# Kernel optimization log

Measured on AMD Instinct MI355X. Metric: run time of the kernel, lower is better.

Reference implementation:

```python
import jax, jax.numpy as jnp
import numpy as np

N = 50000        # nodes
E = 800000       # edges
F_IN = 16        # num_features
F_EDGE = 8       # num_edge_features
H = 4            # heads
C = 32           # hidden_dim (per-head out channels)
D = H * C        # 128, node state width
NUM_CLASSES = 5
NEG_SLOPE = 0.2  # PyG GATConv default leaky_relu slope


def setup_inputs() -> dict:
    key = jax.random.key(0)
    ks = jax.random.split(key, 30)
    def w(k, shape):
        return jax.random.normal(k, shape, dtype=jnp.float32) * 0.05
    return {
        "x": jax.random.normal(ks[0], (N, F_IN), dtype=jnp.float32),
        "edge_index": jax.random.randint(ks[1], (2, E), 0, N),
        "edge_attr": jax.random.normal(ks[2], (E, F_EDGE), dtype=jnp.float32),
        # edge_encoder: Linear(F_EDGE->C), ReLU, Linear(C->H)
        "ee_w1": w(ks[3], (C, F_EDGE)), "ee_b1": jnp.zeros((C,), jnp.float32),
        "ee_w2": w(ks[4], (H, C)),      "ee_b2": jnp.zeros((H,), jnp.float32),
        # input_proj: Linear(F_IN -> D)
        "proj_w": w(ks[5], (D, F_IN)), "proj_b": jnp.zeros((D,), jnp.float32),
        # conv1: GATConv(F_IN, C, heads=H, edge_dim=H, concat=True)
        "c1_lin": w(ks[6], (D, F_IN)),
        "c1_att_src": w(ks[7], (H, C)), "c1_att_dst": w(ks[8], (H, C)),
        "c1_lin_edge": w(ks[9], (D, H)), "c1_att_edge": w(ks[10], (H, C)),
        "c1_bias": jnp.zeros((D,), jnp.float32),
        # conv2: GATConv(D, C, heads=H, edge_dim=H, concat=True)
        "c2_lin": w(ks[11], (D, D)),
        "c2_att_src": w(ks[12], (H, C)), "c2_att_dst": w(ks[13], (H, C)),
        "c2_lin_edge": w(ks[14], (D, H)), "c2_att_edge": w(ks[15], (H, C)),
        "c2_bias": jnp.zeros((D,), jnp.float32),
        # layer norms
        "n1_g": jnp.ones((D,), jnp.float32), "n1_b": jnp.zeros((D,), jnp.float32),
        "n2_g": jnp.ones((D,), jnp.float32), "n2_b": jnp.zeros((D,), jnp.float32),
        # jk_proj: Linear(3D -> D)
        "jk_w": w(ks[16], (D, 3 * D)), "jk_b": jnp.zeros((D,), jnp.float32),
        # classifier: Linear(D -> NUM_CLASSES)
        "cls_w": w(ks[17], (NUM_CLASSES, D)), "cls_b": jnp.zeros((NUM_CLASSES,), jnp.float32),
    }


def _layer_norm(h, g, b, eps=1e-5):
    mu = jnp.mean(h, axis=-1, keepdims=True)
    var = jnp.var(h, axis=-1, keepdims=True)
    return (h - mu) * jax.lax.rsqrt(var + eps) * g + b


def _gat_conv(x, src, dst, e_attr, lin_w, att_src, att_dst, lin_edge_w, att_edge, bias):
    """PyG GATConv (v1) with edge features, concat=True, eval mode (no dropout)."""
    n = x.shape[0]
    xs = (x @ lin_w.T).reshape(n, H, C)                      # [N,H,C]
    a_src = jnp.einsum('nhc,hc->nh', xs, att_src)            # [N,H]
    a_dst = jnp.einsum('nhc,hc->nh', xs, att_dst)            # [N,H]
    ee = (e_attr @ lin_edge_w.T).reshape(-1, H, C)           # [E,H,C]
    a_edge = jnp.einsum('ehc,hc->eh', ee, att_edge)          # [E,H]
    alpha = jax.nn.leaky_relu(a_src[src] + a_dst[dst] + a_edge, NEG_SLOPE)
    # segment softmax over destination neighborhoods
    amax = jax.ops.segment_max(alpha, dst, num_segments=n)
    ex = jnp.exp(alpha - amax[dst])
    denom = jax.ops.segment_sum(ex, dst, num_segments=n)
    alpha = ex / (denom[dst] + 1e-16)                        # [E,H]
    msg = xs[src] * alpha[:, :, None]                        # [E,H,C]
    out = jax.ops.segment_sum(msg, dst, num_segments=n)      # [N,H,C]
    return out.reshape(n, H * C) + bias


def reference(x, edge_index, edge_attr,
              ee_w1, ee_b1, ee_w2, ee_b2,
              proj_w, proj_b,
              c1_lin, c1_att_src, c1_att_dst, c1_lin_edge, c1_att_edge, c1_bias,
              c2_lin, c2_att_src, c2_att_dst, c2_lin_edge, c2_att_edge, c2_bias,
              n1_g, n1_b, n2_g, n2_b,
              jk_w, jk_b, cls_w, cls_b):
    src, dst = edge_index[0], edge_index[1]
    # edge encoder
    e = jax.nn.relu(edge_attr @ ee_w1.T + ee_b1) @ ee_w2.T + ee_b2   # [E,H]
    h0 = x @ proj_w.T + proj_b                                        # [N,D]
    h1 = _gat_conv(x, src, dst, e, c1_lin, c1_att_src, c1_att_dst,
                   c1_lin_edge, c1_att_edge, c1_bias)
    h1 = _layer_norm(jax.nn.elu(h1) + h0, n1_g, n1_b)
    h2 = _gat_conv(h1, src, dst, e, c2_lin, c2_att_src, c2_att_dst,
                   c2_lin_edge, c2_att_edge, c2_bias)
    h2 = _layer_norm(jax.nn.elu(h2) + h1, n2_g, n2_b)
    h = jnp.concatenate([h0, h1, h2], axis=-1) @ jk_w.T + jk_b
    out = h @ cls_w.T + cls_b
    return jax.nn.log_softmax(out, axis=1)
```

## Files before the change

### kernel.cpp

```cpp
#include <hip/hip_runtime.h>
#include <cstdint>

#define NN 50000
#define NE 800000
#define DPX 6250
#define SLICES 391

using short8  = __attribute__((ext_vector_type(8))) short;
using float4v = __attribute__((ext_vector_type(4))) float;

__device__ __forceinline__ ushort f2bf(float f) {
    uint u = __float_as_uint(f);
    uint r = (u + 0x7fffu + ((u >> 16) & 1u)) >> 16;
    return (ushort)r;
}
__device__ __forceinline__ float bf2f(uint u) {
    return __uint_as_float(u << 16);
}

__global__ __launch_bounds__(256) void k_prep2(const float* __restrict__ le1, const float* __restrict__ ae1,
                                               const float* __restrict__ le2, const float* __restrict__ ae2,
                                               const float* __restrict__ jkw, const float* __restrict__ jkb,
                                               const float* __restrict__ clw, const float* __restrict__ clb,
                                               const float* __restrict__ projw, const float* __restrict__ c1lin,
                                               const float* __restrict__ c2lin,
                                               const float* __restrict__ asrc1, const float* __restrict__ adst1,
                                               float* __restrict__ M, float* __restrict__ CW,
                                               float* __restrict__ cbp,
                                               ushort* __restrict__ w01b, ushort* __restrict__ c2b,
                                               float* __restrict__ Vmat, int* __restrict__ deg)
{
    int idx = blockIdx.x * 256 + threadIdx.x;
    if (idx < NN) deg[idx] = 0;
    if (idx < 32) {
        const float* le = (idx < 16) ? le1 : le2;
        const float* ae = (idx < 16) ? ae1 : ae2;
        int hk = idx & 15, h = hk >> 2, k = hk & 3;
        float s = 0.f;
        for (int c = 0; c < 32; ++c)
            s += le[(h * 32 + c) * 4 + k] * ae[h * 32 + c];
        M[idx] = s;
    } else if (idx < 1952) {
        int o = idx - 32;
        int r = o / 384, c = o - r * 384;
        float s = 0.f;
        for (int k = 0; k < 128; ++k)
            s += clw[r * 128 + k] * jkw[(size_t)k * 384 + c];
        CW[o] = s;
    } else if (idx < 1957) {
        int r = idx - 1952;
        float s = clb[r];
        for (int k = 0; k < 128; ++k)
            s += clw[r * 128 + k] * jkb[k];
        cbp[r] = s;
    } else if (idx >= 2048 && idx < 10240) {
        int o = idx - 2048;
        int r = o >> 5, c = o & 31;
        float v = 0.f;
        if (c < 16) v = (r < 128) ? projw[r * 16 + c] : c1lin[(r - 128) * 16 + c];
        w01b[o] = f2bf(v);
    } else if (idx >= 10240 && idx < 26624) {
        int o = idx - 10240;
        c2b[o] = f2bf(c2lin[o]);
    } else if (idx >= 26624 && idx < 26752) {
        int o = idx - 26624;
        const float* att = (o < 64) ? asrc1 : adst1;
        int oo = o & 63, h = oo >> 4, k = oo & 15;
        float s = 0.f;
        for (int c = 0; c < 32; ++c)
            s += c1lin[(h * 32 + c) * 16 + k] * att[h * 32 + c];
        Vmat[o] = s;
    }
}

__global__ __launch_bounds__(256) void k_att1(const float* __restrict__ x,
                                              const float* __restrict__ V,
                                              float* __restrict__ as_o,
                                              float* __restrict__ ad_o)
{
    __shared__ float sV[128];
    int t = threadIdx.x;
    if (t < 128) sV[t] = V[t];
    __syncthreads();
    int n = blockIdx.x * 256 + t;
    if (n >= NN) return;
    const float4* xr = (const float4*)(x + (size_t)n * 16);
    float4 x0 = xr[0], x1 = xr[1], x2 = xr[2], x3 = xr[3];
    float xv[16] = {x0.x,x0.y,x0.z,x0.w, x1.x,x1.y,x1.z,x1.w,
                    x2.x,x2.y,x2.z,x2.w, x3.x,x3.y,x3.z,x3.w};
    float s[4], d[4];
    #pragma unroll
    for (int h = 0; h < 4; ++h) {
        float ss = 0.f, dd = 0.f;
        #pragma unroll
        for (int k = 0; k < 16; ++k) {
            ss += xv[k] * sV[h * 16 + k];
            dd += xv[k] * sV[64 + h * 16 + k];
        }
        s[h] = ss; d[h] = dd;
    }
    *(float4*)(as_o + (size_t)n * 4) = make_float4(s[0], s[1], s[2], s[3]);
    *(float4*)(ad_o + (size_t)n * 4) = make_float4(d[0], d[1], d[2], d[3]);
}

__global__ __launch_bounds__(256) void k_edge_mlp(const float* __restrict__ ea,
                                                  const float* __restrict__ w1,
                                                  const float* __restrict__ b1,
                                                  const float* __restrict__ w2,
                                                  const float* __restrict__ b2,
                                                  const int* __restrict__ ei,
                                                  const float* __restrict__ Mm,
                                                  const float* __restrict__ as1,
                                                  const float* __restrict__ ad1,
                                                  ushort* __restrict__ exb,
                                                  ushort* __restrict__ ae2)
{
    __shared__ float sw1[256], sb1[32], sw2[128], sb2[4], sM[32];
    int t = threadIdx.x;
    sw1[t] = w1[t];
    if (t < 128) sw2[t] = w2[t];
    if (t < 32)  { sb1[t] = b1[t]; sM[t] = Mm[t]; }
    if (t < 4)   sb2[t] = b2[t];
    __syncthreads();
    int e = blockIdx.x * 256 + t;
    if (e >= NE) return;
    int src = ei[e], dst = ei[NE + e];
    float4 s4 = *(const float4*)(as1 + (size_t)src * 4);
    float4 d4 = *(const float4*)(ad1 + (size_t)dst * 4);
    float4 x0 = *(const float4*)(ea + (size_t)e * 8);
    float4 x1 = *(const float4*)(ea + (size_t)e * 8 + 4);
    float o0 = sb2[0], o1 = sb2[1], o2 = sb2[2], o3 = sb2[3];
    #pragma unroll
    for (int j = 0; j < 32; ++j) {
        const float* w = sw1 + j * 8;
        float s = sb1[j] + w[0]*x0.x + w[1]*x0.y + w[2]*x0.z + w[3]*x0.w
                         + w[4]*x1.x + w[5]*x1.y + w[6]*x1.z + w[7]*x1.w;
        s = fmaxf(s, 0.f);
        o0 += sw2[0*32+j] * s; o1 += sw2[1*32+j] * s;
        o2 += sw2[2*32+j] * s; o3 += sw2[3*32+j] * s;
    }
    float sa[4] = {s4.x, s4.y, s4.z, s4.w};
    float da[4] = {d4.x, d4.y, d4.z, d4.w};
    ushort exq[4], a2q[4];
    #pragma unroll
    for (int h = 0; h < 4; ++h) {
        float ae1 = sM[h*4+0]*o0 + sM[h*4+1]*o1 + sM[h*4+2]*o2 + sM[h*4+3]*o3;
        float al = sa[h] + da[h] + ae1;
        al = al > 0.f ? al : 0.2f * al;
        exq[h] = f2bf(__expf(al));
        a2q[h] = f2bf(sM[16+h*4+0]*o0 + sM[16+h*4+1]*o1 + sM[16+h*4+2]*o2 + sM[16+h*4+3]*o3);
    }
    *(uint2*)(exb + (size_t)e * 4) =
        make_uint2((uint)exq[0] | ((uint)exq[1] << 16), (uint)exq[2] | ((uint)exq[3] << 16));
    *(uint2*)(ae2 + (size_t)e * 4) =
        make_uint2((uint)a2q[0] | ((uint)a2q[1] << 16), (uint)a2q[2] | ((uint)a2q[3] << 16));
}

__global__ __launch_bounds__(256) void k_hist8(const int* __restrict__ ei, int* __restrict__ deg)
{
    int grp = blockIdx.x & 7;
    int base = (blockIdx.x >> 3) * 2048 + threadIdx.x;
    #pragma unroll
    for (int k = 0; k < 8; ++k) {
        int e = base + k * 256;
        if (e < NE) {
            int dst = ei[NE + e];
            if (dst / DPX == grp) atomicAdd(&deg[dst], 1);
        }
    }
}

__global__ __launch_bounds__(256) void k_scan_blk(const int* __restrict__ deg,
                                                  int* __restrict__ loc,
                                                  int* __restrict__ bsum)
{
    __shared__ int tmp[256];
    int t = threadIdx.x;
    int i = blockIdx.x * 256 + t;
    int v = (i < NN) ? deg[i] : 0;
    tmp[t] = v;
    __syncthreads();
    #pragma unroll
    for (int o = 1; o < 256; o <<= 1) {
        int add = (t >= o) ? tmp[t - o] : 0;
        __syncthreads();
        tmp[t] += add;
        __syncthreads();
    }
    if (i < NN) loc[i] = tmp[t] - v;
    if (t == 255) bsum[blockIdx.x] = tmp[255];
}

__global__ __launch_bounds__(256) void k_scan_top(const int* __restrict__ bsum,
                                                  int* __restrict__ bcarry,
                                                  int* __restrict__ total_out, int nb)
{
    __shared__ int tmp[256];
    int t = threadIdx.x;
    int v = (t < nb) ? bsum[t] : 0;
    tmp[t] = v;
    __syncthreads();
    #pragma unroll
    for (int o = 1; o < 256; o <<= 1) {
        int add = (t >= o) ? tmp[t - o] : 0;
        __syncthreads();
        tmp[t] += add;
        __syncthreads();
    }
    if (t < nb) bcarry[t] = tmp[t] - v;
    if (t == 255) *total_out = tmp[255];
}

__global__ __launch_bounds__(256) void k_scan_add(const int* __restrict__ loc,
                                                  const int* __restrict__ bcarry,
                                                  int* __restrict__ off,
                                                  int* __restrict__ cur)
{
    int i = blockIdx.x * 256 + threadIdx.x;
    if (i < NN) {
        int o = loc[i] + bcarry[blockIdx.x];
        off[i] = o;
        cur[i] = o;
    }
}

__global__ __launch_bounds__(256) void k_scatter8(const int* __restrict__ ei,
                                                  int* __restrict__ cursor,
                                                  int2* __restrict__ csr2)
{
    int grp = blockIdx.x & 7;
    int base = (blockIdx.x >> 3) * 2048 + threadIdx.x;
    #pragma unroll
    for (int k = 0; k < 8; ++k) {
        int e = base + k * 256;
        if (e < NE) {
            int dst = ei[NE + e];
            if (dst / DPX == grp) {
                int src = ei[e];
                int p = atomicAdd(&cursor[dst], 1);
                csr2[p] = make_int2(src, e);
            }
        }
    }
}

__global__ __launch_bounds__(256) void k_gemm1(const float* __restrict__ x,
                                               const ushort* __restrict__ w01,
                                               const float* __restrict__ pbias,
                                               ushort* __restrict__ hcatb,
                                               ushort* __restrict__ xs, int M)
{
    int t = threadIdx.x;
    int wv = t >> 6, lane = t & 63;
    int quad = lane >> 4, r16 = lane & 15;
    int m0 = blockIdx.x * 128 + wv * 32;
    int ar0 = m0 + r16;      if (ar0 >= M) ar0 = M - 1;
    int ar1 = m0 + 16 + r16; if (ar1 >= M) ar1 = M - 1;
    short8 a0 = (short8){0,0,0,0,0,0,0,0}, a1 = a0;
    if (quad < 2) {
        const float* p0 = x + (size_t)ar0 * 16 + quad * 8;
        const float* p1 = x + (size_t)ar1 * 16 + quad * 8;
        float4 u0 = *(const float4*)p0, u1 = *(const float4*)(p0 + 4);
        float4 v0 = *(const float4*)p1, v1 = *(const float4*)(p1 + 4);
        a0[0]=(short)f2bf(u0.x); a0[1]=(short)f2bf(u0.y); a0[2]=(short)f2bf(u0.z); a0[3]=(short)f2bf(u0.w);
        a0[4]=(short)f2bf(u1.x); a0[5]=(short)f2bf(u1.y); a0[6]=(short)f2bf(u1.z); a0[7]=(short)f2bf(u1.w);
        a1[0]=(short)f2bf(v0.x); a1[1]=(short)f2bf(v0.y); a1[2]=(short)f2bf(v0.z); a1[3]=(short)f2bf(v0.w);
        a1[4]=(short)f2bf(v1.x); a1[5]=(short)f2bf(v1.y); a1[6]=(short)f2bf(v1.z); a1[7]=(short)f2bf(v1.w);
    }
    float4v acc[2][16];
    #pragma unroll
    for (int i = 0; i < 2; ++i)
        #pragma unroll
        for (int j = 0; j < 16; ++j) acc[i][j] = (float4v){0.f, 0.f, 0.f, 0.f};
    #pragma unroll
    for (int nt = 0; nt < 16; ++nt) {
        short8 b = *(const short8*)(w01 + (size_t)(nt * 16 + r16) * 32 + quad * 8);
        acc[0][nt] = __builtin_amdgcn_mfma_f32_16x16x32_bf16(a0, b, acc[0][nt], 0, 0, 0);
        acc[1][nt] = __builtin_amdgcn_mfma_f32_16x16x32_bf16(a1, b, acc[1][nt], 0, 0, 0);
    }
    #pragma unroll
    for (int rt = 0; rt < 2; ++rt) {
        #pragma unroll
        for (int nt = 0; nt < 16; ++nt) {
            int col = (nt & 7) * 16 + r16;
            float bv = (nt < 8) ? pbias[col] : 0.f;
            #pragma unroll
            for (int r = 0; r < 4; ++r) {
                int row = m0 + rt * 16 + quad * 4 + r;
                if (row < M) {
                    float v = acc[rt][nt][r] + bv;
                    if (nt < 8) hcatb[(size_t)row * 384 + col] = f2bf(v);
                    else        xs[(size_t)row * 128 + col] = f2bf(v);
                }
            }
        }
    }
}

__global__ __launch_bounds__(256) void k_gemm2(const ushort* __restrict__ A,
                                               const ushort* __restrict__ W,
                                               const float* __restrict__ atts,
                                               const float* __restrict__ attd,
                                               ushort* __restrict__ xs,
                                               float* __restrict__ as_o,
                                               float* __restrict__ ad_o, int M)
{
    __shared__ float sAs[128], sAd[128];
    int t = threadIdx.x;
    if (t < 128) { sAs[t] = atts[t]; sAd[t] = attd[t]; }
    __syncthreads();
    int wv = t >> 6, lane = t & 63;
    int quad = lane >> 4, r16 = lane & 15;
    int m0 = blockIdx.x * 128 + wv * 32;
    float4v acc[2][8];
    #pragma unroll
    for (int i = 0; i < 2; ++i)
        #pragma unroll
        for (int j = 0; j < 8; ++j) acc[i][j] = (float4v){0.f, 0.f, 0.f, 0.f};
    int ar0 = m0 + r16;      if (ar0 >= M) ar0 = M - 1;
    int ar1 = m0 + 16 + r16; if (ar1 >= M) ar1 = M - 1;
    const ushort* a0p = A + (size_t)ar0 * 384 + quad * 8;
    const ushort* a1p = A + (size_t)ar1 * 384 + quad * 8;
    const ushort* wp  = W + (size_t)r16 * 128 + quad * 8;
    #pragma unroll
    for (int k0 = 0; k0 < 128; k0 += 32) {
        short8 a0 = *(const short8*)(a0p + k0);
        short8 a1 = *(const short8*)(a1p + k0);
        #pragma unroll
        for (int nt = 0; nt < 8; ++nt) {
            short8 b = *(const short8*)(wp + (size_t)(nt * 16) * 128 + k0);
            acc[0][nt] = __builtin_amdgcn_mfma_f32_16x16x32_bf16(a0, b, acc[0][nt], 0, 0, 0);
            acc[1][nt] = __builtin_amdgcn_mfma_f32_16x16x32_bf16(a1, b, acc[1][nt], 0, 0, 0);
        }
    }
    #pragma unroll
    for (int rt = 0; rt < 2; ++rt) {
        #pragma unroll
        for (int nt = 0; nt < 8; ++nt) {
            int col = nt * 16 + r16;
            #pragma unroll
            for (int r = 0; r < 4; ++r) {
                int row = m0 + rt * 16 + quad * 4 + r;
                if (row < M)
                    xs[(size_t)row * 128 + col] = f2bf(acc[rt][nt][r]);
            }
        }
        #pragma unroll
        for (int r = 0; r < 4; ++r) {
            int row = m0 + rt * 16 + quad * 4 + r;
            float sh[4], dh[4];
            #pragma unroll
            for (int h = 0; h < 4; ++h) {
                int cA = h * 32 + r16, cB = cA + 16;
                sh[h] = acc[rt][2*h][r] * sAs[cA] + acc[rt][2*h+1][r] * sAs[cB];
                dh[h] = acc[rt][2*h][r] * sAd[cA] + acc[rt][2*h+1][r] * sAd[cB];
            }
            #pragma unroll
            for (int o = 1; o < 16; o <<= 1) {
                #pragma unroll
                for (int h = 0; h < 4; ++h) {
                    sh[h] += __shfl_xor(sh[h], o, 64);
                    dh[h] += __shfl_xor(dh[h], o, 64);
                }
            }
            if (r16 == 0 && row < M) {
                *(float4*)(as_o + (size_t)row * 4) = make_float4(sh[0], sh[1], sh[2], sh[3]);
                *(float4*)(ad_o + (size_t)row * 4) = make_float4(dh[0], dh[1], dh[2], dh[3]);
            }
        }
    }
}

__global__ __launch_bounds__(256) void k_edge_soft2(const int* __restrict__ ei,
                                                    const float* __restrict__ as_in,
                                                    const float* __restrict__ ad_in,
                                                    const ushort* __restrict__ ae2,
                                                    ushort* __restrict__ exb)
{
    int e = blockIdx.x * 256 + threadIdx.x;
    if (e >= NE) return;
    int src = ei[e], dst = ei[NE + e];
    float4 s4 = *(const float4*)(as_in + (size_t)src * 4);
    float4 d4 = *(const float4*)(ad_in + (size_t)dst * 4);
    uint2 aq = *(const uint2*)(ae2 + (size_t)e * 4);
    float av[4] = {bf2f(aq.x & 0xffffu), bf2f(aq.x >> 16), bf2f(aq.y & 0xffffu), bf2f(aq.y >> 16)};
    float sa[4] = {s4.x, s4.y, s4.z, s4.w};
    float da[4] = {d4.x, d4.y, d4.z, d4.w};
    ushort exq[4];
    #pragma unroll
    for (int h = 0; h < 4; ++h) {
        float al = sa[h] + da[h] + av[h];
        al = al > 0.f ? al : 0.2f * al;
        exq[h] = f2bf(__expf(al));
    }
    *(uint2*)(exb + (size_t)e * 4) =
        make_uint2((uint)exq[0] | ((uint)exq[1] << 16), (uint)exq[2] | ((uint)exq[3] << 16));
}

__global__ __launch_bounds__(256) void k_agg2(const int* __restrict__ off,
                                              const int2* __restrict__ csr2,
                                              const ushort* __restrict__ exb,
                                              const ushort* __restrict__ xs,
                                              const float* __restrict__ bias,
                                              const ushort* __restrict__ residb,
                                              const float* __restrict__ g,
                                              const float* __restrict__ bln,
                                              ushort* __restrict__ outb)
{
    int wave = threadIdx.x >> 6;
    int lane = threadIdx.x & 63;
    int n = blockIdx.x * 4 + wave;
    if (n >= NN) return;
    int i0 = off[n], i1 = off[n + 1];
    int c0 = lane * 2;
    int h = lane >> 4;
    float a0 = 0.f, a1 = 0.f, den = 0.f;
    int i = i0;
    for (; i + 4 <= i1; i += 4) {
        int2 se0 = csr2[i], se1 = csr2[i+1], se2 = csr2[i+2], se3 = csr2[i+3];
        float w0 = bf2f(exb[(size_t)se0.y * 4 + h]);
        float w1 = bf2f(exb[(size_t)se1.y * 4 + h]);
        float w2 = bf2f(exb[(size_t)se2.y * 4 + h]);
        float w3 = bf2f(exb[(size_t)se3.y * 4 + h]);
        uint p0 = *(const uint*)(xs + (size_t)se0.x * 128 + c0);
        uint p1 = *(const uint*)(xs + (size_t)se1.x * 128 + c0);
        uint p2 = *(const uint*)(xs + (size_t)se2.x * 128 + c0);
        uint p3 = *(const uint*)(xs + (size_t)se3.x * 128 + c0);
        a0 = fmaf(bf2f(p0 & 0xffffu), w0, a0); a1 = fmaf(bf2f(p0 >> 16), w0, a1);
        a0 = fmaf(bf2f(p1 & 0xffffu), w1, a0); a1 = fmaf(bf2f(p1 >> 16), w1, a1);
        a0 = fmaf(bf2f(p2 & 0xffffu), w2, a0); a1 = fmaf(bf2f(p2 >> 16), w2, a1);
        a0 = fmaf(bf2f(p3 & 0xffffu), w3, a0); a1 = fmaf(bf2f(p3 >> 16), w3, a1);
        den += (w0 + w1) + (w2 + w3);
    }
    for (; i < i1; ++i) {
        int2 se0 = csr2[i];
        float w0 = bf2f(exb[(size_t)se0.y * 4 + h]);
        uint p0 = *(const uint*)(xs + (size_t)se0.x * 128 + c0);
        a0 = fmaf(bf2f(p0 & 0xffffu), w0, a0);
        a1 = fmaf(bf2f(p0 >> 16), w0, a1);
        den += w0;
    }
    float inv = 1.f / (den + 1e-16f);
    float v0 = a0 * inv + bias[c0];
    float v1 = a1 * inv + bias[c0 + 1];
    v0 = v0 > 0.f ? v0 : (__expf(v0) - 1.f);
    v1 = v1 > 0.f ? v1 : (__expf(v1) - 1.f);
    uint rp = *(const uint*)(residb + (size_t)n * 384 + c0);
    float r0 = v0 + bf2f(rp & 0xffffu);
    float r1 = v1 + bf2f(rp >> 16);
    float ssum = r0 + r1, ssq = r0 * r0 + r1 * r1;
    #pragma unroll
    for (int o = 1; o < 64; o <<= 1) {
        ssum += __shfl_xor(ssum, o, 64);
        ssq  += __shfl_xor(ssq, o, 64);
    }
    float mu = ssum * (1.f / 128.f);
    float var = ssq * (1.f / 128.f) - mu * mu;
    float rs = rsqrtf(var + 1e-5f);
    float o0 = (r0 - mu) * rs * g[c0] + bln[c0];
    float o1 = (r1 - mu) * rs * g[c0 + 1] + bln[c0 + 1];
    uint pk = (uint)f2bf(o0) | ((uint)f2bf(o1) << 16);
    *(uint*)(outb + (size_t)n * 384 + c0) = pk;
}

__global__ __launch_bounds__(256) void k_cls(const ushort* __restrict__ hcatb,
                                             const float* __restrict__ CW,
                                             const float* __restrict__ cbp,
                                             float* __restrict__ out)
{
    __shared__ float sCW[1920], scb[5];
    int t = threadIdx.x;
    for (int i = t; i < 1920; i += 256) sCW[i] = CW[i];
    if (t < 5) scb[t] = cbp[t];
    __syncthreads();
    int n = blockIdx.x * 256 + t;
    if (n >= NN) return;
    float acc[5] = {scb[0], scb[1], scb[2], scb[3], scb[4]};
    const uint2* hr = (const uint2*)(hcatb + (size_t)n * 384);
    #pragma unroll 4
    for (int q = 0; q < 96; ++q) {
        uint2 p = hr[q];
        float v0 = bf2f(p.x & 0xffffu), v1 = bf2f(p.x >> 16);
        float v2 = bf2f(p.y & 0xffffu), v3 = bf2f(p.y >> 16);
        #pragma unroll
        for (int o = 0; o < 5; ++o) {
            const float* w = sCW + o * 384 + q * 4;
            acc[o] += v0*w[0] + v1*w[1] + v2*w[2] + v3*w[3];
        }
    }
    float m = acc[0];
    #pragma unroll
    for (int o = 1; o < 5; ++o) m = fmaxf(m, acc[o]);
    float sum = 0.f;
    #pragma unroll
    for (int o = 0; o < 5; ++o) sum += __expf(acc[o] - m);
    float lse = __logf(sum) + m;
    float* op = out + (size_t)n * 5;
    #pragma unroll
    for (int o = 0; o < 5; ++o) op[o] = acc[o] - lse;
}

extern "C" void kernel_launch(void* const* d_in, const int* in_sizes, int n_in,
                              void* d_out, int out_size, void* d_ws, size_t ws_size,
                              hipStream_t stream)
{
    (void)in_sizes; (void)n_in; (void)out_size; (void)ws_size;
    const float* x        = (const float*)d_in[0];
    const int*   ei       = (const int*)d_in[1];
    const float* eattr    = (const float*)d_in[2];
    const float* ee_w1    = (const float*)d_in[3];
    const float* ee_b1    = (const float*)d_in[4];
    const float* ee_w2    = (const float*)d_in[5];
    const float* ee_b2    = (const float*)d_in[6];
    const float* proj_w   = (const float*)d_in[7];
    const float* proj_b   = (const float*)d_in[8];
    const float* c1_lin   = (const float*)d_in[9];
    const float* c1_asrc  = (const float*)d_in[10];
    const float* c1_adst  = (const float*)d_in[11];
    const float* c1_ledge = (const float*)d_in[12];
    const float* c1_aedge = (const float*)d_in[13];
    const float* c1_bias  = (const float*)d_in[14];
    const float* c2_lin   = (const float*)d_in[15];
    const float* c2_asrc  = (const float*)d_in[16];
    const float* c2_adst  = (const float*)d_in[17];
    const float* c2_ledge = (const float*)d_in[18];
    const float* c2_aedge = (const float*)d_in[19];
    const float* c2_bias  = (const float*)d_in[20];
    const float* n1_g     = (const float*)d_in[21];
    const float* n1_b     = (const float*)d_in[22];
    const float* n2_g     = (const float*)d_in[23];
    const float* n2_b     = (const float*)d_in[24];
    const float* jk_w     = (const float*)d_in[25];
    const float* jk_b     = (const float*)d_in[26];
    const float* cls_w    = (const float*)d_in[27];
    const float* cls_b    = (const float*)d_in[28];
    float* out = (float*)d_out;
    float* ws  = (float*)d_ws;

    const size_t oM   = 0;
    const size_t oCW  = 64;
    const size_t oCB  = 1984;
    const size_t oV   = 2048;
    const size_t oEX  = 2176;
    const size_t oAE2 = oEX + (size_t)NE * 2;
    const size_t oHB  = oAE2 + (size_t)NE * 2;
    const size_t oXS  = oHB + (size_t)NN * 192;
    const size_t oWB  = oXS + (size_t)NN * 64;
    const size_t oAS  = oWB + 12288;
    const size_t oAD  = oAS + (size_t)NN * 4;
    const size_t oI   = oAD + (size_t)NN * 4;

    float*  Mmat  = ws + oM;
    float*  CW    = ws + oCW;
    float*  cbp   = ws + oCB;
    float*  Vmat  = ws + oV;
    ushort* exb   = (ushort*)(ws + oEX);
    ushort* ae2b  = (ushort*)(ws + oAE2);
    ushort* hcatb = (ushort*)(ws + oHB);
    ushort* xs    = (ushort*)(ws + oXS);
    ushort* w01b  = (ushort*)(ws + oWB);
    ushort* c2b   = w01b + 8192;
    float*  as_b  = ws + oAS;
    float*  ad_b  = ws + oAD;
    int*    ip    = (int*)(ws + oI);
    int*    deg   = ip;
    int*    loc   = ip + NN;
    int*    off   = ip + 2 * NN;
    int*    cur   = ip + 3 * NN + 16;
    int*    bsum  = ip + 4 * NN + 16;
    int*    bcar  = ip + 4 * NN + 272;
    int2*   csr2  = (int2*)(ip + 4 * NN + 528);

    const int EB  = (NE + 255) / 256;
    const int NB  = (NN + 255) / 256;
    const int GB  = (NN + 127) / 128;
    const int WB2 = (NN + 3) / 4;
    const int PB  = SLICES * 8;

    k_prep2<<<NB, 256, 0, stream>>>(c1_ledge, c1_aedge, c2_ledge, c2_aedge,
                                    jk_w, jk_b, cls_w, cls_b,
                                    proj_w, c1_lin, c2_lin, c1_asrc, c1_adst,
                                    Mmat, CW, cbp, w01b, c2b, Vmat, deg);
    k_hist8<<<PB, 256, 0, stream>>>(ei, deg);
    k_scan_blk<<<NB, 256, 0, stream>>>(deg, loc, bsum);
    k_scan_top<<<1, 256, 0, stream>>>(bsum, bcar, off + NN, NB);
    k_scan_add<<<NB, 256, 0, stream>>>(loc, bcar, off, cur);
    k_scatter8<<<PB, 256, 0, stream>>>(ei, cur, csr2);

    k_att1<<<NB, 256, 0, stream>>>(x, Vmat, as_b, ad_b);
    k_edge_mlp<<<EB, 256, 0, stream>>>(eattr, ee_w1, ee_b1, ee_w2, ee_b2, ei,
                                       Mmat, as_b, ad_b, exb, ae2b);

    k_gemm1<<<GB, 256, 0, stream>>>(x, w01b, proj_b, hcatb, xs, NN);

    k_agg2<<<WB2, 256, 0, stream>>>(off, csr2, exb, xs, c1_bias, hcatb,
                                    n1_g, n1_b, hcatb + 128);

    k_gemm2<<<GB, 256, 0, stream>>>(hcatb + 128, c2b, c2_asrc, c2_adst,
                                    xs, as_b, ad_b, NN);
    k_edge_soft2<<<EB, 256, 0, stream>>>(ei, as_b, ad_b, ae2b, exb);
    k_agg2<<<WB2, 256, 0, stream>>>(off, csr2, exb, xs, c2_bias, hcatb + 128,
                                    n2_g, n2_b, hcatb + 256);

    k_cls<<<NB, 256, 0, stream>>>(hcatb, CW, cbp, out);
}
```

Before: 394.5 us.

## Pre-bin edges by destination range before CSR histogram and placement

```diff
diff --git a/kernel.cpp b/kernel.cpp
--- a/kernel.cpp
+++ b/kernel.cpp
@@ -4,7 +4,7 @@
 #define NN 50000
 #define NE 800000
 #define DPX 6250
-#define SLICES 391
+#define BINCAP 163840
 
 using short8  = __attribute__((ext_vector_type(8))) short;
 using float4v = __attribute__((ext_vector_type(4))) float;
@@ -28,10 +28,12 @@
                                                float* __restrict__ M, float* __restrict__ CW,
                                                float* __restrict__ cbp,
                                                ushort* __restrict__ w01b, ushort* __restrict__ c2b,
-                                               float* __restrict__ Vmat, int* __restrict__ deg)
+                                               float* __restrict__ Vmat, int* __restrict__ deg,
+                                               int* __restrict__ binCnt)
 {
     int idx = blockIdx.x * 256 + threadIdx.x;
     if (idx < NN) deg[idx] = 0;
+    if (idx >= NN && idx < NN + 8) binCnt[idx - NN] = 0;
     if (idx < 32) {
         const float* le = (idx < 16) ? le1 : le2;
         const float* ae = (idx < 16) ? ae1 : ae2;
@@ -103,6 +105,138 @@
     *(float4*)(ad_o + (size_t)n * 4) = make_float4(d[0], d[1], d[2], d[3]);
 }
 
+__global__ __launch_bounds__(256) void k_binA(const int* __restrict__ ei,
+                                              int* __restrict__ binCnt,
+                                              uint2* __restrict__ binbuf)
+{
+    __shared__ uint sd_l[2048];
+    __shared__ uint e_l[2048];
+    __shared__ int bcnt[8], bbase[8], gbase[8];
+    int t = threadIdx.x;
+    if (t < 8) bcnt[t] = 0;
+    __syncthreads();
+    int base = blockIdx.x * 2048;
+    int cnt = NE - base; if (cnt > 2048) cnt = 2048;
+    uint mysd[8], myb[8], myslot[8]; int mye[8]; int nloc = 0;
+    #pragma unroll
+    for (int k = 0; k < 8; ++k) {
+        int j = t + k * 256;
+        if (j < cnt) {
+            int e = base + j;
+            int src = ei[e], dst = ei[NE + e];
+            uint b = (uint)dst / DPX;
+            uint slot = atomicAdd(&bcnt[b], 1);
+            mysd[nloc] = ((uint)src << 16) | (uint)dst;
+            myb[nloc] = b; myslot[nloc] = slot; mye[nloc] = e;
+            ++nloc;
+        }
+    }
+    __syncthreads();
+    if (t == 0) {
+        int run = 0;
+        #pragma unroll
+        for (int b = 0; b < 8; ++b) { bbase[b] = run; run += bcnt[b]; }
+    }
+    __syncthreads();
+    if (t < 8) gbase[t] = atomicAdd(&binCnt[t], bcnt[t]);
+    __syncthreads();
+    for (int k = 0; k < nloc; ++k) {
+        int pos = bbase[myb[k]] + (int)myslot[k];
+        sd_l[pos] = mysd[k];
+        e_l[pos]  = (uint)mye[k] | (myb[k] << 24);
+    }
+    __syncthreads();
+    for (int j = t; j < cnt; j += 256) {
+        uint ep = e_l[j];
+        uint b = ep >> 24;
+        int gi = gbase[b] + (j - bbase[b]);
+        binbuf[(size_t)b * BINCAP + gi] = make_uint2(sd_l[j], ep & 0xFFFFFFu);
+    }
+}
+
+__global__ __launch_bounds__(256) void k_histB(const uint2* __restrict__ binbuf,
+                                               const int* __restrict__ binCnt,
+                                               int* __restrict__ deg)
+{
+    int b = blockIdx.x & 7;
+    int nb = binCnt[b];
+    const uint2* seg = binbuf + (size_t)b * BINCAP;
+    int stride = (gridDim.x >> 3) * 256;
+    for (int i = (blockIdx.x >> 3) * 256 + threadIdx.x; i < nb; i += stride)
+        atomicAdd(&deg[seg[i].x & 0xFFFFu], 1);
+}
+
+__global__ __launch_bounds__(256) void k_scan_blk(const int* __restrict__ deg,
+                                                  int* __restrict__ loc,
+                                                  int* __restrict__ bsum)
+{
+    __shared__ int tmp[256];
+    int t = threadIdx.x;
+    int i = blockIdx.x * 256 + t;
+    int v = (i < NN) ? deg[i] : 0;
+    tmp[t] = v;
+    __syncthreads();
+    #pragma unroll
+    for (int o = 1; o < 256; o <<= 1) {
+        int add = (t >= o) ? tmp[t - o] : 0;
+        __syncthreads();
+        tmp[t] += add;
+        __syncthreads();
+    }
+    if (i < NN) loc[i] = tmp[t] - v;
+    if (t == 255) bsum[blockIdx.x] = tmp[255];
+}
+
+__global__ __launch_bounds__(256) void k_scan_top(const int* __restrict__ bsum,
+                                                  int* __restrict__ bcarry,
+                                                  int* __restrict__ total_out, int nb)
+{
+    __shared__ int tmp[256];
+    int t = threadIdx.x;
+    int v = (t < nb) ? bsum[t] : 0;
+    tmp[t] = v;
+    __syncthreads();
+    #pragma unroll
+    for (int o = 1; o < 256; o <<= 1) {
+        int add = (t >= o) ? tmp[t - o] : 0;
+        __syncthreads();
+        tmp[t] += add;
+        __syncthreads();
+    }
+    if (t < nb) bcarry[t] = tmp[t] - v;
+    if (t == 255) *total_out = tmp[255];
+}
+
+__global__ __launch_bounds__(256) void k_scan_add(const int* __restrict__ loc,
+                                                  const int* __restrict__ bcarry,
+                                                  int* __restrict__ off,
+                                                  int* __restrict__ cur)
+{
+    int i = blockIdx.x * 256 + threadIdx.x;
+    if (i < NN) {
+        int o = loc[i] + bcarry[blockIdx.x];
+        off[i] = o;
+        cur[i] = o;
+    }
+}
+
+__global__ __launch_bounds__(256) void k_placeB(const uint2* __restrict__ binbuf,
+                                                const int* __restrict__ binCnt,
+                                                int* __restrict__ cur,
+                                                int2* __restrict__ csr2)
+{
+    int b = blockIdx.x & 7;
+    int nb = binCnt[b];
+    const uint2* seg = binbuf + (size_t)b * BINCAP;
+    int stride = (gridDim.x >> 3) * 256;
+    for (int i = (blockIdx.x >> 3) * 256 + threadIdx.x; i < nb; i += stride) {
+        uint2 v = seg[i];
+        int dst = (int)(v.x & 0xFFFFu), src = (int)(v.x >> 16);
+        int p = atomicAdd(&cur[dst], 1);
+        csr2[p] = make_int2(src, (int)v.y);
+    }
+}
+
 __global__ __launch_bounds__(256) void k_edge_mlp(const float* __restrict__ ea,
                                                   const float* __restrict__ w1,
                                                   const float* __restrict__ b1,
@@ -154,94 +288,6 @@
         make_uint2((uint)exq[0] | ((uint)exq[1] << 16), (uint)exq[2] | ((uint)exq[3] << 16));
     *(uint2*)(ae2 + (size_t)e * 4) =
         make_uint2((uint)a2q[0] | ((uint)a2q[1] << 16), (uint)a2q[2] | ((uint)a2q[3] << 16));
-}
-
-__global__ __launch_bounds__(256) void k_hist8(const int* __restrict__ ei, int* __restrict__ deg)
-{
-    int grp = blockIdx.x & 7;
-    int base = (blockIdx.x >> 3) * 2048 + threadIdx.x;
-    #pragma unroll
-    for (int k = 0; k < 8; ++k) {
-        int e = base + k * 256;
-        if (e < NE) {
-            int dst = ei[NE + e];
-            if (dst / DPX == grp) atomicAdd(&deg[dst], 1);
-        }
-    }
-}
-
-__global__ __launch_bounds__(256) void k_scan_blk(const int* __restrict__ deg,
-                                                  int* __restrict__ loc,
-                                                  int* __restrict__ bsum)
-{
-    __shared__ int tmp[256];
-    int t = threadIdx.x;
-    int i = blockIdx.x * 256 + t;
-    int v = (i < NN) ? deg[i] : 0;
-    tmp[t] = v;
-    __syncthreads();
-    #pragma unroll
-    for (int o = 1; o < 256; o <<= 1) {
-        int add = (t >= o) ? tmp[t - o] : 0;
-        __syncthreads();
-        tmp[t] += add;
-        __syncthreads();
-    }
-    if (i < NN) loc[i] = tmp[t] - v;
-    if (t == 255) bsum[blockIdx.x] = tmp[255];
-}
-
-__global__ __launch_bounds__(256) void k_scan_top(const int* __restrict__ bsum,
-                                                  int* __restrict__ bcarry,
-                                                  int* __restrict__ total_out, int nb)
-{
-    __shared__ int tmp[256];
-    int t = threadIdx.x;
-    int v = (t < nb) ? bsum[t] : 0;
-    tmp[t] = v;
-    __syncthreads();
-    #pragma unroll
-    for (int o = 1; o < 256; o <<= 1) {
-        int add = (t >= o) ? tmp[t - o] : 0;
-        __syncthreads();
-        tmp[t] += add;
-        __syncthreads();
-    }
-    if (t < nb) bcarry[t] = tmp[t] - v;
-    if (t == 255) *total_out = tmp[255];
-}
-
-__global__ __launch_bounds__(256) void k_scan_add(const int* __restrict__ loc,
-                                                  const int* __restrict__ bcarry,
-                                                  int* __restrict__ off,
-                                                  int* __restrict__ cur)
-{
-    int i = blockIdx.x * 256 + threadIdx.x;
-    if (i < NN) {
-        int o = loc[i] + bcarry[blockIdx.x];
-        off[i] = o;
-        cur[i] = o;
-    }
-}
-
-__global__ __launch_bounds__(256) void k_scatter8(const int* __restrict__ ei,
-                                                  int* __restrict__ cursor,
-                                                  int2* __restrict__ csr2)
-{
-    int grp = blockIdx.x & 7;
-    int base = (blockIdx.x >> 3) * 2048 + threadIdx.x;
-    #pragma unroll
-    for (int k = 0; k < 8; ++k) {
-        int e = base + k * 256;
-        if (e < NE) {
-            int dst = ei[NE + e];
-            if (dst / DPX == grp) {
-                int src = ei[e];
-                int p = atomicAdd(&cursor[dst], 1);
-                csr2[p] = make_int2(src, e);
-            }
-        }
-    }
 }
 
 __global__ __launch_bounds__(256) void k_gemm1(const float* __restrict__ x,
@@ -416,21 +462,39 @@
     int h = lane >> 4;
     float a0 = 0.f, a1 = 0.f, den = 0.f;
     int i = i0;
+    for (; i + 8 <= i1; i += 8) {
+        int2 se[8];
+        #pragma unroll
+        for (int j = 0; j < 8; ++j) se[j] = csr2[i + j];
+        float w[8];
+        #pragma unroll
+        for (int j = 0; j < 8; ++j) w[j] = bf2f(exb[(size_t)se[j].y * 4 + h]);
+        uint p[8];
+        #pragma unroll
+        for (int j = 0; j < 8; ++j) p[j] = *(const uint*)(xs + (size_t)se[j].x * 128 + c0);
+        #pragma unroll
+        for (int j = 0; j < 8; ++j) {
+            a0 = fmaf(bf2f(p[j] & 0xffffu), w[j], a0);
+            a1 = fmaf(bf2f(p[j] >> 16), w[j], a1);
+            den += w[j];
+        }
+    }
     for (; i + 4 <= i1; i += 4) {
-        int2 se0 = csr2[i], se1 = csr2[i+1], se2 = csr2[i+2], se3 = csr2[i+3];
-        float w0 = bf2f(exb[(size_t)se0.y * 4 + h]);
-        float w1 = bf2f(exb[(size_t)se1.y * 4 + h]);
-        float w2 = bf2f(exb[(size_t)se2.y * 4 + h]);
-        float w3 = bf2f(exb[(size_t)se3.y * 4 + h]);
-        uint p0 = *(const uint*)(xs + (size_t)se0.x * 128 + c0);
-        uint p1 = *(const uint*)(xs + (size_t)se1.x * 128 + c0);
-        uint p2 = *(const uint*)(xs + (size_t)se2.x * 128 + c0);
-        uint p3 = *(const uint*)(xs + (size_t)se3.x * 128 + c0);
-        a0 = fmaf(bf2f(p0 & 0xffffu), w0, a0); a1 = fmaf(bf2f(p0 >> 16), w0, a1);
-        a0 = fmaf(bf2f(p1 & 0xffffu), w1, a0); a1 = fmaf(bf2f(p1 >> 16), w1, a1);
-        a0 = fmaf(bf2f(p2 & 0xffffu), w2, a0); a1 = fmaf(bf2f(p2 >> 16), w2, a1);
-        a0 = fmaf(bf2f(p3 & 0xffffu), w3, a0); a1 = fmaf(bf2f(p3 >> 16), w3, a1);
-        den += (w0 + w1) + (w2 + w3);
+        int2 se[4];
+        #pragma unroll
+        for (int j = 0; j < 4; ++j) se[j] = csr2[i + j];
+        float w[4];
+        #pragma unroll
+        for (int j = 0; j < 4; ++j) w[j] = bf2f(exb[(size_t)se[j].y * 4 + h]);
+        uint p[4];
+        #pragma unroll
+        for (int j = 0; j < 4; ++j) p[j] = *(const uint*)(xs + (size_t)se[j].x * 128 + c0);
+        #pragma unroll
+        for (int j = 0; j < 4; ++j) {
+            a0 = fmaf(bf2f(p[j] & 0xffffu), w[j], a0);
+            a1 = fmaf(bf2f(p[j] >> 16), w[j], a1);
+            den += w[j];
+        }
     }
     for (; i < i1; ++i) {
         int2 se0 = csr2[i];
@@ -563,29 +627,33 @@
     float*  as_b  = ws + oAS;
     float*  ad_b  = ws + oAD;
     int*    ip    = (int*)(ws + oI);
-    int*    deg   = ip;
-    int*    loc   = ip + NN;
-    int*    off   = ip + 2 * NN;
-    int*    cur   = ip + 3 * NN + 16;
-    int*    bsum  = ip + 4 * NN + 16;
-    int*    bcar  = ip + 4 * NN + 272;
-    int2*   csr2  = (int2*)(ip + 4 * NN + 528);
+    int*    deg    = ip;
+    int*    loc    = ip + NN;
+    int*    off    = ip + 2 * NN;
+    int*    cur    = ip + 3 * NN + 16;
+    int*    bsum   = ip + 4 * NN + 16;
+    int*    bcar   = ip + 4 * NN + 272;
+    int*    binCnt = ip + 4 * NN + 528;
+    int2*   csr2   = (int2*)(ip + 4 * NN + 544);
+    uint2*  binbuf = (uint2*)(ip + 4 * NN + 544 + 2 * (size_t)NE);
 
     const int EB  = (NE + 255) / 256;
     const int NB  = (NN + 255) / 256;
     const int GB  = (NN + 127) / 128;
     const int WB2 = (NN + 3) / 4;
-    const int PB  = SLICES * 8;
+    const int BB  = (NE + 2047) / 2048;
+    const int PB  = 512;
 
     k_prep2<<<NB, 256, 0, stream>>>(c1_ledge, c1_aedge, c2_ledge, c2_aedge,
                                     jk_w, jk_b, cls_w, cls_b,
                                     proj_w, c1_lin, c2_lin, c1_asrc, c1_adst,
-                                    Mmat, CW, cbp, w01b, c2b, Vmat, deg);
-    k_hist8<<<PB, 256, 0, stream>>>(ei, deg);
+                                    Mmat, CW, cbp, w01b, c2b, Vmat, deg, binCnt);
+    k_binA<<<BB, 256, 0, stream>>>(ei, binCnt, binbuf);
+    k_histB<<<PB, 256, 0, stream>>>(binbuf, binCnt, deg);
     k_scan_blk<<<NB, 256, 0, stream>>>(deg, loc, bsum);
     k_scan_top<<<1, 256, 0, stream>>>(bsum, bcar, off + NN, NB);
     k_scan_add<<<NB, 256, 0, stream>>>(loc, bcar, off, cur);
-    k_scatter8<<<PB, 256, 0, stream>>>(ei, cur, csr2);
+    k_placeB<<<PB, 256, 0, stream>>>(binbuf, binCnt, cur, csr2);
 
     k_att1<<<NB, 256, 0, stream>>>(x, Vmat, as_b, ad_b);
     k_edge_mlp<<<EB, 256, 0, stream>>>(eattr, ee_w1, ee_b1, ee_w2, ee_b2, ei,
```

After: 400.9 us. About the same (+1.6%).

## Pack edge softmax weights into CSR entries to remove random gathers in aggregation

Applied to the files above, without the earlier changes.

```diff
diff --git a/kernel.cpp b/kernel.cpp
--- a/kernel.cpp
+++ b/kernel.cpp
@@ -225,8 +225,9 @@
 }
 
 __global__ __launch_bounds__(256) void k_scatter8(const int* __restrict__ ei,
+                                                  const ushort* __restrict__ exb,
                                                   int* __restrict__ cursor,
-                                                  int2* __restrict__ csr2)
+                                                  int4* __restrict__ csr4)
 {
     int grp = blockIdx.x & 7;
     int base = (blockIdx.x >> 3) * 2048 + threadIdx.x;
@@ -237,8 +238,9 @@
             int dst = ei[NE + e];
             if (dst / DPX == grp) {
                 int src = ei[e];
+                uint2 ex = *(const uint2*)(exb + (size_t)e * 4);
                 int p = atomicAdd(&cursor[dst], 1);
-                csr2[p] = make_int2(src, e);
+                csr4[p] = make_int4((src << 16) | dst, e, (int)ex.x, (int)ex.y);
             }
         }
     }
@@ -371,18 +373,19 @@
     }
 }
 
-__global__ __launch_bounds__(256) void k_edge_soft2(const int* __restrict__ ei,
-                                                    const float* __restrict__ as_in,
-                                                    const float* __restrict__ ad_in,
-                                                    const ushort* __restrict__ ae2,
-                                                    ushort* __restrict__ exb)
-{
-    int e = blockIdx.x * 256 + threadIdx.x;
-    if (e >= NE) return;
-    int src = ei[e], dst = ei[NE + e];
+__global__ __launch_bounds__(256) void k_soft2csr(int4* __restrict__ csr4,
+                                                  const float* __restrict__ as_in,
+                                                  const float* __restrict__ ad_in,
+                                                  const ushort* __restrict__ ae2)
+{
+    int i = blockIdx.x * 256 + threadIdx.x;
+    if (i >= NE) return;
+    int4 en = csr4[i];
+    uint sd = (uint)en.x;
+    int src = (int)(sd >> 16), dst = (int)(sd & 0xffffu);
     float4 s4 = *(const float4*)(as_in + (size_t)src * 4);
     float4 d4 = *(const float4*)(ad_in + (size_t)dst * 4);
-    uint2 aq = *(const uint2*)(ae2 + (size_t)e * 4);
+    uint2 aq = *(const uint2*)(ae2 + (size_t)en.y * 4);
     float av[4] = {bf2f(aq.x & 0xffffu), bf2f(aq.x >> 16), bf2f(aq.y & 0xffffu), bf2f(aq.y >> 16)};
     float sa[4] = {s4.x, s4.y, s4.z, s4.w};
     float da[4] = {d4.x, d4.y, d4.z, d4.w};
@@ -393,13 +396,13 @@
         al = al > 0.f ? al : 0.2f * al;
         exq[h] = f2bf(__expf(al));
     }
-    *(uint2*)(exb + (size_t)e * 4) =
-        make_uint2((uint)exq[0] | ((uint)exq[1] << 16), (uint)exq[2] | ((uint)exq[3] << 16));
+    en.z = (int)((uint)exq[0] | ((uint)exq[1] << 16));
+    en.w = (int)((uint)exq[2] | ((uint)exq[3] << 16));
+    csr4[i] = en;
 }
 
 __global__ __launch_bounds__(256) void k_agg2(const int* __restrict__ off,
-                                              const int2* __restrict__ csr2,
-                                              const ushort* __restrict__ exb,
+                                              const int4* __restrict__ csr4,
                                               const ushort* __restrict__ xs,
                                               const float* __restrict__ bias,
                                               const ushort* __restrict__ residb,
@@ -414,31 +417,51 @@
     int i0 = off[n], i1 = off[n + 1];
     int c0 = lane * 2;
     int h = lane >> 4;
+    int hsel = h >> 1, hsh = (h & 1) << 4;
     float a0 = 0.f, a1 = 0.f, den = 0.f;
     int i = i0;
+    for (; i + 8 <= i1; i += 8) {
+        int4 en[8];
+        #pragma unroll
+        for (int j = 0; j < 8; ++j) en[j] = csr4[i + j];
+        uint p[8];
+        #pragma unroll
+        for (int j = 0; j < 8; ++j)
+            p[j] = *(const uint*)(xs + (size_t)((uint)en[j].x >> 16) * 128 + c0);
+        #pragma unroll
+        for (int j = 0; j < 8; ++j) {
+            uint exsel = (uint)(hsel ? en[j].w : en[j].z);
+            float w = bf2f((exsel >> hsh) & 0xffffu);
+            a0 = fmaf(bf2f(p[j] & 0xffffu), w, a0);
+            a1 = fmaf(bf2f(p[j] >> 16), w, a1);
+            den += w;
+        }
+    }
     for (; i + 4 <= i1; i += 4) {
-        int2 se0 = csr2[i], se1 = csr2[i+1], se2 = csr2[i+2], se3 = csr2[i+3];
-        float w0 = bf2f(exb[(size_t)se0.y * 4 + h]);
-        float w1 = bf2f(exb[(size_t)se1.y * 4 + h]);
-        float w2 = bf2f(exb[(size_t)se2.y * 4 + h]);
-        float w3 = bf2f(exb[(size_t)se3.y * 4 + h]);
-        uint p0 = *(const uint*)(xs + (size_t)se0.x * 128 + c0);
-        uint p1 = *(const uint*)(xs + (size_t)se1.x * 128 + c0);
-        uint p2 = *(const uint*)(xs + (size_t)se2.x * 128 + c0);
-        uint p3 = *(const uint*)(xs + (size_t)se3.x * 128 + c0);
-        a0 = fmaf(bf2f(p0 & 0xffffu), w0, a0); a1 = fmaf(bf2f(p0 >> 16), w0, a1);
-        a0 = fmaf(bf2f(p1 & 0xffffu), w1, a0); a1 = fmaf(bf2f(p1 >> 16), w1, a1);
-        a0 = fmaf(bf2f(p2 & 0xffffu), w2, a0); a1 = fmaf(bf2f(p2 >> 16), w2, a1);
-        a0 = fmaf(bf2f(p3 & 0xffffu), w3, a0); a1 = fmaf(bf2f(p3 >> 16), w3, a1);
-        den += (w0 + w1) + (w2 + w3);
+        int4 en[4];
+        #pragma unroll
+        for (int j = 0; j < 4; ++j) en[j] = csr4[i + j];
+        uint p[4];
+        #pragma unroll
+        for (int j = 0; j < 4; ++j)
+            p[j] = *(const uint*)(xs + (size_t)((uint)en[j].x >> 16) * 128 + c0);
+        #pragma unroll
+        for (int j = 0; j < 4; ++j) {
+            uint exsel = (uint)(hsel ? en[j].w : en[j].z);
+            float w = bf2f((exsel >> hsh) & 0xffffu);
+            a0 = fmaf(bf2f(p[j] & 0xffffu), w, a0);
+            a1 = fmaf(bf2f(p[j] >> 16), w, a1);
+            den += w;
+        }
     }
     for (; i < i1; ++i) {
-        int2 se0 = csr2[i];
-        float w0 = bf2f(exb[(size_t)se0.y * 4 + h]);
-        uint p0 = *(const uint*)(xs + (size_t)se0.x * 128 + c0);
-        a0 = fmaf(bf2f(p0 & 0xffffu), w0, a0);
-        a1 = fmaf(bf2f(p0 >> 16), w0, a1);
-        den += w0;
+        int4 en = csr4[i];
+        uint p0 = *(const uint*)(xs + (size_t)((uint)en.x >> 16) * 128 + c0);
+        uint exsel = (uint)(hsel ? en.w : en.z);
+        float w = bf2f((exsel >> hsh) & 0xffffu);
+        a0 = fmaf(bf2f(p0 & 0xffffu), w, a0);
+        a1 = fmaf(bf2f(p0 >> 16), w, a1);
+        den += w;
     }
     float inv = 1.f / (den + 1e-16f);
     float v0 = a0 * inv + bias[c0];
@@ -569,7 +592,7 @@
     int*    cur   = ip + 3 * NN + 16;
     int*    bsum  = ip + 4 * NN + 16;
     int*    bcar  = ip + 4 * NN + 272;
-    int2*   csr2  = (int2*)(ip + 4 * NN + 528);
+    int4*   csr4  = (int4*)(ip + 4 * NN + 544);
 
     const int EB  = (NE + 255) / 256;
     const int NB  = (NN + 255) / 256;
@@ -581,25 +604,24 @@
                                     jk_w, jk_b, cls_w, cls_b,
                                     proj_w, c1_lin, c2_lin, c1_asrc, c1_adst,
                                     Mmat, CW, cbp, w01b, c2b, Vmat, deg);
+    k_att1<<<NB, 256, 0, stream>>>(x, Vmat, as_b, ad_b);
+    k_edge_mlp<<<EB, 256, 0, stream>>>(eattr, ee_w1, ee_b1, ee_w2, ee_b2, ei,
+                                       Mmat, as_b, ad_b, exb, ae2b);
     k_hist8<<<PB, 256, 0, stream>>>(ei, deg);
     k_scan_blk<<<NB, 256, 0, stream>>>(deg, loc, bsum);
     k_scan_top<<<1, 256, 0, stream>>>(bsum, bcar, off + NN, NB);
     k_scan_add<<<NB, 256, 0, stream>>>(loc, bcar, off, cur);
-    k_scatter8<<<PB, 256, 0, stream>>>(ei, cur, csr2);
-
-    k_att1<<<NB, 256, 0, stream>>>(x, Vmat, as_b, ad_b);
-    k_edge_mlp<<<EB, 256, 0, stream>>>(eattr, ee_w1, ee_b1, ee_w2, ee_b2, ei,
-                                       Mmat, as_b, ad_b, exb, ae2b);
+    k_scatter8<<<PB, 256, 0, stream>>>(ei, exb, cur, csr4);
 
     k_gemm1<<<GB, 256, 0, stream>>>(x, w01b, proj_b, hcatb, xs, NN);
 
-    k_agg2<<<WB2, 256, 0, stream>>>(off, csr2, exb, xs, c1_bias, hcatb,
+    k_agg2<<<WB2, 256, 0, stream>>>(off, csr4, xs, c1_bias, hcatb,
                                     n1_g, n1_b, hcatb + 128);
 
     k_gemm2<<<GB, 256, 0, stream>>>(hcatb + 128, c2b, c2_asrc, c2_adst,
                                     xs, as_b, ad_b, NN);
-    k_edge_soft2<<<EB, 256, 0, stream>>>(ei, as_b, ad_b, ae2b, exb);
-    k_agg2<<<WB2, 256, 0, stream>>>(off, csr2, exb, xs, c2_bias, hcatb + 128,
+    k_soft2csr<<<EB, 256, 0, stream>>>(csr4, as_b, ad_b, ae2b);
+    k_agg2<<<WB2, 256, 0, stream>>>(off, csr4, xs, c2_bias, hcatb + 128,
                                     n2_g, n2_b, hcatb + 256);
 
     k_cls<<<NB, 256, 0, stream>>>(hcatb, CW, cbp, out);
```

Measured after the change: 393.4 us. Within noise of the previous version (-0.3%).
